# Optimization experiments

Hardware: AMD Instinct MI355X
Metric: run time of the kernel (lower is better)

Reference implementation:

```python
import jax, jax.numpy as jnp
import numpy as np

B, M, K = 32768, 8192, 16
EPS = 1e-5  # torch BatchNorm1d default


def _bn_relu(x, g, b):
    # training-mode batch norm (biased variance), matching torch BatchNorm1d forward
    m = x.mean(0)
    v = x.var(0)
    return jax.nn.relu(g * (x - m) * jax.lax.rsqrt(v + EPS) + b)


def _forward(pos, mc, mv, w1, b1, w2, b2, w3, b3, w4, b4, w5, b5, w6, b6,
             g1, be1, g2, be2, g3, be3, g4, be4, g5, be5, k):
    # squared pairwise distances [B, M]; same ordering as L2 norm used by torch.sort
    d2 = (pos * pos).sum(1, keepdims=True) + (mc * mc).sum(1)[None, :] - 2.0 * (pos @ mc.T)
    _, idx = jax.lax.top_k(-d2, k)                     # k nearest indices [B, k]
    nb = jnp.concatenate([mc[idx], mv[idx]], axis=-1)  # [B, k, 4] = (coord, value) per neighbor
    knn_feat = jnp.concatenate([pos, nb.reshape(pos.shape[0], k * 4)], axis=1)  # [B, 2+4k]
    x = _bn_relu(knn_feat @ w1 + b1, g1, be1)
    x = _bn_relu(x @ w2 + b2, g2, be2)
    x = _bn_relu(x @ w3 + b3, g3, be3)
    x = _bn_relu(x @ w4 + b4, g4, be4)
    x = _bn_relu(x @ w5 + b5, g5, be5)  # dropout = identity (eval mode)
    x = x @ w6 + b6
    return x, knn_feat


def setup_inputs() -> dict:
    key = jax.random.key(0)
    ks = jax.random.split(key, 32)
    d_in = 2 + K * 4
    dims = [(d_in, 128), (128, 256), (256, 512), (512, 128), (128, 64), (64, 2)]
    inp = {
        "pos": jax.random.normal(ks[0], (B, 2), jnp.float32),
        "measure_coords": jax.random.normal(ks[1], (M, 2), jnp.float32),
        "measure_vals": jax.random.normal(ks[2], (M, 2), jnp.float32),
    }
    for i, (fi, fo) in enumerate(dims, 1):
        inp[f"w{i}"] = jax.random.normal(ks[2 + 2 * i], (fi, fo), jnp.float32) / np.float32(np.sqrt(fi))
        inp[f"b{i}"] = jnp.zeros((fo,), jnp.float32)
    for i, n in enumerate([128, 256, 512, 128, 64], 1):
        inp[f"g{i}"] = jnp.ones((n,), jnp.float32)
        inp[f"be{i}"] = jnp.zeros((n,), jnp.float32)
    inp["k"] = K
    return inp


def reference(pos, measure_coords, measure_vals, w1, b1, w2, b2, w3, b3, w4, b4,
              w5, b5, w6, b6, g1, be1, g2, be2, g3, be3, g4, be4, g5, be5, k):
    return _forward(pos, measure_coords, measure_vals, w1, b1, w2, b2, w3, b3, w4,
                    b4, w5, b5, w6, b6, g1, be1, g2, be2, g3, be3, g4, be4, g5, be5, k)
```

## Files before the change

kernel.cpp:

```cpp
#include <hip/hip_runtime.h>

typedef unsigned short u16;
typedef unsigned int   u32;
typedef __attribute__((ext_vector_type(8))) short bf16x8;
typedef __attribute__((ext_vector_type(4))) float f32x4;

#define B_ROWS 32768
#define EPS_BN 1e-5f

__device__ __forceinline__ u16 f2bf(float f) {
  u32 u = __float_as_uint(f);
  u32 r = (u + 0x7FFFu + ((u >> 16) & 1u)) >> 16;
  return (u16)r;
}
__device__ __forceinline__ float bf2f(u16 h) {
  return __uint_as_float(((u32)h) << 16);
}

__device__ __forceinline__ float dcalc(float px, float py, float sp, float mx, float my) {
#pragma clang fp contract(off)
  float sm   = mx * mx + my * my;
  float pm   = px * mx;
  float dot  = __builtin_fmaf(py, my, pm);
  float spsm = sp + sm;
  return __builtin_fmaf(dot, -2.0f, spsm);
}
__device__ __forceinline__ float dcalc2(float px, float py, float sp, float mx, float my,
                                        float sm) {
#pragma clang fp contract(off)
  float pm   = px * mx;
  float dot  = __builtin_fmaf(py, my, pm);
  float spsm = sp + sm;
  return __builtin_fmaf(dot, -2.0f, spsm);
}
__device__ __forceinline__ float smcalc(float mx, float my) {
#pragma clang fp contract(off)
  return mx * mx + my * my;
}
__device__ __forceinline__ float spcalc(float px, float py) {
#pragma clang fp contract(off)
  return px * px + py * py;
}
#define MED3 __builtin_amdgcn_fmed3f

__device__ __forceinline__ int nth_set_bit(unsigned long long m, int n) {
  u32 w = (u32)m;
  int base = 0;
  int c = __popc(w);
  if (n >= c) { n -= c; w = (u32)(m >> 32); base = 32; }
  int p = __popc(w & 0xFFFFu); if (n >= p) { n -= p; w >>= 16; base += 16; }
  p = __popc(w & 0xFFu);       if (n >= p) { n -= p; w >>= 8;  base += 8; }
  p = __popc(w & 0xFu);        if (n >= p) { n -= p; w >>= 4;  base += 4; }
  p = __popc(w & 0x3u);        if (n >= p) { n -= p; w >>= 2;  base += 2; }
  p = (int)(w & 1u);           if (n >= p) { base += 1; }
  return base;
}

__device__ __forceinline__ float sel8(const float a[8], int j) {
  float x01 = (j & 1) ? a[1] : a[0];
  float x23 = (j & 1) ? a[3] : a[2];
  float x45 = (j & 1) ? a[5] : a[4];
  float x67 = (j & 1) ? a[7] : a[6];
  float xl  = (j & 2) ? x23 : x01;
  float xh  = (j & 2) ? x67 : x45;
  return (j & 4) ? xh : xl;
}

__global__ __launch_bounds__(256, 4)
void knn_kernel(const float2* __restrict__ pos, const float2* __restrict__ mc,
                const float2* __restrict__ mv, float* __restrict__ knn_out,
                u16* __restrict__ X0)
{
  __shared__ float tv[32 * 130];
  __shared__ float tstS[32];
  __shared__ int   qcnt[32];

  const int t = threadIdx.x;
  const int g = t >> 6;
  const int s = t & 63;
  const int q0 = blockIdx.x * 32;

  float px[8], py[8], sp[8];
#pragma unroll
  for (int j = 0; j < 8; ++j) {
    float2 p = pos[q0 + g * 8 + j];
    px[j] = p.x; py[j] = p.y; sp[j] = spcalc(p.x, p.y);
  }

  const float4* mc4 = (const float4*)mc;
  const int b4 = s * 64;

  float z0[8], z1[8];
#pragma unroll
  for (int j = 0; j < 8; ++j) { z0[j] = __builtin_inff(); z1[j] = __builtin_inff(); }

  float4 cur = mc4[b4];
  for (int i = 0; i < 64; ++i) {
    float4 nxt = mc4[b4 + ((i + 1) & 63)];
    float smA = smcalc(cur.x, cur.y);
    float smB = smcalc(cur.z, cur.w);
#pragma unroll
    for (int j = 0; j < 8; ++j) {
      float dA = dcalc2(px[j], py[j], sp[j], cur.x, cur.y, smA);
      z1[j] = MED3(z0[j], dA, z1[j]); z0[j] = fminf(z0[j], dA);
      float dB = dcalc2(px[j], py[j], sp[j], cur.z, cur.w, smB);
      z1[j] = MED3(z0[j], dB, z1[j]); z0[j] = fminf(z0[j], dB);
    }
    cur = nxt;
  }
#pragma unroll
  for (int j = 0; j < 8; ++j) {
    float2 zz; zz.x = z0[j]; zz.y = z1[j];
    *(float2*)(&tv[(g * 8 + j) * 130 + s * 2]) = zz;
  }
  __syncthreads();

  if (t < 32) {
    float ch[16];
#pragma unroll
    for (int j = 0; j < 16; ++j) ch[j] = __builtin_inff();
    for (int k = 0; k < 128; ++k) {
      float v = tv[t * 130 + k];
#pragma unroll
      for (int j = 15; j >= 1; --j) ch[j] = MED3(ch[j-1], v, ch[j]);
      ch[0] = fminf(ch[0], v);
    }
    tstS[t] = ch[15];
    qcnt[t] = 0;
  }
  __syncthreads();
  float Tq[8];
#pragma unroll
  for (int j = 0; j < 8; ++j) Tq[j] = tstS[g * 8 + j];
  __syncthreads();

  unsigned long long am[8];
#pragma unroll
  for (int j = 0; j < 8; ++j) am[j] = __ballot(z0[j] <= Tq[j]);
  int total = 0;
#pragma unroll
  for (int j = 0; j < 8; ++j) total += __popcll(am[j]);

  u16* qcand = (u16*)tv;
  for (int t0 = s; t0 < total; t0 += 64) {
    int rem = t0, jq = 0, sl = -1;
#pragma unroll
    for (int jj = 0; jj < 8; ++jj) {
      if (sl < 0) {
        int c = __popcll(am[jj]);
        if (rem < c) { sl = nth_set_bit(am[jj], rem); jq = jj; }
        else rem -= c;
      }
    }
    float qx = sel8(px, jq), qy = sel8(py, jq);
    float qs = sel8(sp, jq), qT = sel8(Tq, jq);
    const int qrow = g * 8 + jq;
    const int bpt = sl * 128;
    const float4* mbase = mc4 + sl * 64;
#pragma unroll 4
    for (int i = 0; i < 64; ++i) {
      float4 c2 = mbase[i];
      float smA = smcalc(c2.x, c2.y);
      float smB = smcalc(c2.z, c2.w);
      float dA = dcalc2(qx, qy, qs, c2.x, c2.y, smA);
      float dB = dcalc2(qx, qy, qs, c2.z, c2.w, smB);
      if (dA <= qT) {
        int o = atomicAdd(&qcnt[qrow], 1);
        if (o < 64) qcand[qrow * 64 + o] = (u16)(bpt + 2 * i);
      }
      if (dB <= qT) {
        int o = atomicAdd(&qcnt[qrow], 1);
        if (o < 64) qcand[qrow * 64 + o] = (u16)(bpt + 2 * i + 1);
      }
    }
  }
  __syncthreads();

  if (t < 32) {
    const int q = q0 + t;
    float2 p = pos[q];
    const float sq = spcalc(p.x, p.y);
    int cnt = qcnt[t]; if (cnt > 64) cnt = 64;
    float fd[16]; int fi[16];
#pragma unroll
    for (int j = 0; j < 16; ++j) { fd[j] = __builtin_inff(); fi[j] = 0x7fffffff; }
    for (int j = 0; j < cnt; ++j) {
      int ci = qcand[t * 64 + j];
      float2 m = mc[ci];
      float d = dcalc(p.x, p.y, sq, m.x, m.y);
      bool cc = (d < fd[15]) || (d == fd[15] && ci < fi[15]);
      if (cc) {
#pragma unroll
        for (int k = 15; k >= 1; --k) {
          bool cm = (d < fd[k-1]) || (d == fd[k-1] && ci < fi[k-1]);
          if (cc) {
            if (cm) { fd[k] = fd[k-1]; fi[k] = fi[k-1]; }
            else    { fd[k] = d;       fi[k] = ci;      }
          }
          cc = cm;
        }
        if (cc) { fd[0] = d; fi[0] = ci; }
      }
    }
    float* orow = knn_out + (size_t)q * 66;
    u16*   xrow = X0 + (size_t)q * 96;
    orow[0] = p.x; orow[1] = p.y;
    xrow[0] = f2bf(p.x); xrow[1] = f2bf(p.y);
#pragma unroll
    for (int j = 0; j < 16; ++j) {
      int ci = fi[j];
      float2 m = mc[ci], v = mv[ci];
      orow[2 + 4*j + 0] = m.x; orow[2 + 4*j + 1] = m.y;
      orow[2 + 4*j + 2] = v.x; orow[2 + 4*j + 3] = v.y;
      xrow[2 + 4*j + 0] = f2bf(m.x); xrow[2 + 4*j + 1] = f2bf(m.y);
      xrow[2 + 4*j + 2] = f2bf(v.x); xrow[2 + 4*j + 3] = f2bf(v.y);
    }
#pragma unroll
    for (int c = 66; c < 96; ++c) xrow[c] = 0;
  }
}

__global__ __launch_bounds__(256)
void prep_wt_all(const float* __restrict__ w1, const float* __restrict__ w2,
                 const float* __restrict__ w3, const float* __restrict__ w4,
                 const float* __restrict__ w5,
                 u16* __restrict__ wt1, u16* __restrict__ wt2, u16* __restrict__ wt3,
                 u16* __restrict__ wt4, u16* __restrict__ wt5)
{
  const int l = blockIdx.y;
  const float* w; u16* wt; int K, N, Kp;
  if (l == 0)      { w = w1; wt = wt1; K = 66;  N = 128; Kp = 96;  }
  else if (l == 1) { w = w2; wt = wt2; K = 128; N = 256; Kp = 128; }
  else if (l == 2) { w = w3; wt = wt3; K = 256; N = 512; Kp = 256; }
  else if (l == 3) { w = w4; wt = wt4; K = 512; N = 128; Kp = 512; }
  else             { w = w5; wt = wt5; K = 128; N = 64;  Kp = 128; }
  int i = blockIdx.x * 256 + threadIdx.x;
  if (i >= N * Kp) return;
  int n = i / Kp, kp = i - n * Kp;
  float v = (kp < K) ? w[(size_t)kp * N + n] : 0.0f;
  wt[i] = f2bf(v);
}

template<int BN, bool FUSE>
__global__ __launch_bounds__(256)
void gemm_bn_kernel(const u16* __restrict__ X, int Kw,
                    const u16* __restrict__ WT,
                    const float* __restrict__ bias,
                    const float* __restrict__ psum, const float* __restrict__ psq,
                    const float* __restrict__ gw,   const float* __restrict__ bw,
                    u16* __restrict__ Z, int N,
                    float* __restrict__ csum, float* __restrict__ csq)
{
  constexpr int BM = 128;
  constexpr int AST = 40;
  __shared__ u16 Ash[BM * AST];
  __shared__ u16 Bsh[BN * AST];
  __shared__ float redS[4][BN];
  __shared__ float redQ[4][BN];
  __shared__ float scA[512];
  __shared__ float ttA[512];

  const int t = threadIdx.x;
  const int wave = t >> 6;
  const int lane = t & 63;
  const int lr = lane & 15;
  const int qd = lane >> 4;
  const int m0 = blockIdx.x * BM;
  const int n0 = blockIdx.y * BN;

  if (FUSE) {
    const float invB = 1.0f / 32768.0f;
    for (int c = t; c < Kw; c += 256) {
      float mean = psum[c] * invB;
      float var  = __fmaf_rn(-mean, mean, psq[c] * invB);
      float sc   = gw[c] * rsqrtf(var + EPS_BN);
      scA[c] = sc;
      ttA[c] = __fmaf_rn(-mean, sc, bw[c]);
    }
    __syncthreads();
  }

  f32x4 acc[2][BN / 16];
#pragma unroll
  for (int a = 0; a < 2; ++a)
#pragma unroll
    for (int b = 0; b < BN / 16; ++b) {
      acc[a][b][0] = 0.f; acc[a][b][1] = 0.f; acc[a][b][2] = 0.f; acc[a][b][3] = 0.f;
    }

  const int sr = t >> 2;
  const int sk = (t & 3) * 8;

  for (int k0 = 0; k0 < Kw; k0 += 32) {
#pragma unroll
    for (int rr = 0; rr < 2; ++rr) {
      int r = sr + rr * 64;
      uint4 g = *(const uint4*)(&X[(size_t)(m0 + r) * Kw + k0 + sk]);
      if (FUSE) {
        u32 w[4] = {g.x, g.y, g.z, g.w};
        u32 o[4];
#pragma unroll
        for (int e = 0; e < 4; ++e) {
          int kk = k0 + sk + 2 * e;
          float lo = bf2f((u16)(w[e] & 0xffffu));
          float hi = bf2f((u16)(w[e] >> 16));
          float yl = fmaxf(__fmaf_rn(lo, scA[kk],     ttA[kk]),     0.0f);
          float yh = fmaxf(__fmaf_rn(hi, scA[kk + 1], ttA[kk + 1]), 0.0f);
          o[e] = (u32)f2bf(yl) | ((u32)f2bf(yh) << 16);
        }
        g.x = o[0]; g.y = o[1]; g.z = o[2]; g.w = o[3];
      }
      *(uint4*)(&Ash[r * AST + sk]) = g;
    }
    if (BN == 128) {
#pragma unroll
      for (int rr = 0; rr < 2; ++rr) {
        int n = sr + rr * 64;
        *(uint4*)(&Bsh[n * AST + sk]) =
            *(const uint4*)(&WT[(size_t)(n0 + n) * Kw + k0 + sk]);
      }
    } else {
      int n = sr;
      *(uint4*)(&Bsh[n * AST + sk]) =
          *(const uint4*)(&WT[(size_t)(n0 + n) * Kw + k0 + sk]);
    }
    __syncthreads();
    bf16x8 af0 = *(const bf16x8*)(&Ash[(wave * 32 + lr) * AST + qd * 8]);
    bf16x8 af1 = *(const bf16x8*)(&Ash[(wave * 32 + 16 + lr) * AST + qd * 8]);
#pragma unroll
    for (int ct = 0; ct < BN / 16; ++ct) {
      bf16x8 bfr = *(const bf16x8*)(&Bsh[(ct * 16 + lr) * AST + qd * 8]);
      acc[0][ct] = __builtin_amdgcn_mfma_f32_16x16x32_bf16(af0, bfr, acc[0][ct], 0, 0, 0);
      acc[1][ct] = __builtin_amdgcn_mfma_f32_16x16x32_bf16(af1, bfr, acc[1][ct], 0, 0, 0);
    }
    __syncthreads();
  }

#pragma unroll
  for (int ct = 0; ct < BN / 16; ++ct) {
    int cg = n0 + ct * 16 + lr;
    float bv = bias[cg];
    float s = 0.f, sqv = 0.f;
#pragma unroll
    for (int rt = 0; rt < 2; ++rt) {
#pragma unroll
      for (int r = 0; r < 4; ++r) {
        float z = acc[rt][ct][r] + bv;
        int row = m0 + wave * 32 + rt * 16 + qd * 4 + r;
        Z[(size_t)row * N + cg] = f2bf(z);
        s += z;
        sqv = __fmaf_rn(z, z, sqv);
      }
    }
    s   += __shfl_xor(s, 16);   s   += __shfl_xor(s, 32);
    sqv += __shfl_xor(sqv, 16); sqv += __shfl_xor(sqv, 32);
    if (qd == 0) { redS[wave][ct * 16 + lr] = s; redQ[wave][ct * 16 + lr] = sqv; }
  }
  __syncthreads();
  if (t < BN) {
    float s  = redS[0][t] + redS[1][t] + redS[2][t] + redS[3][t];
    float sv = redQ[0][t] + redQ[1][t] + redQ[2][t] + redQ[3][t];
    atomicAdd(&csum[n0 + t], s);
    atomicAdd(&csq[n0 + t], sv);
  }
}

__global__ __launch_bounds__(256)
void gemv6_kernel(const u16* __restrict__ Z5, const float* __restrict__ w6,
                  const float* __restrict__ b6,
                  const float* __restrict__ psum, const float* __restrict__ psq,
                  const float* __restrict__ gw,   const float* __restrict__ bw,
                  float* __restrict__ out)
{
  __shared__ float wsh[128];
  __shared__ float scs[64];
  __shared__ float tts[64];
  const int t = threadIdx.x;
  if (t < 128) wsh[t] = w6[t];
  if (t < 64) {
    const float invB = 1.0f / 32768.0f;
    float mean = psum[t] * invB;
    float var  = __fmaf_rn(-mean, mean, psq[t] * invB);
    float sc   = gw[t] * rsqrtf(var + EPS_BN);
    scs[t] = sc;
    tts[t] = __fmaf_rn(-mean, sc, bw[t]);
  }
  __syncthreads();
  const int q = blockIdx.x * 256 + t;
  const uint4* xv = (const uint4*)(Z5 + (size_t)q * 64);
  float a0 = 0.f, a1 = 0.f;
#pragma unroll
  for (int cc = 0; cc < 8; ++cc) {
    uint4 pk = xv[cc];
    u32 u[4] = {pk.x, pk.y, pk.z, pk.w};
#pragma unroll
    for (int uu = 0; uu < 4; ++uu) {
      int k = cc * 8 + uu * 2;
      float z0 = bf2f((u16)(u[uu] & 0xffffu));
      float z1 = bf2f((u16)(u[uu] >> 16));
      float x0 = fmaxf(__fmaf_rn(z0, scs[k],     tts[k]),     0.0f);
      float x1 = fmaxf(__fmaf_rn(z1, scs[k + 1], tts[k + 1]), 0.0f);
      x0 = bf2f(f2bf(x0));
      x1 = bf2f(f2bf(x1));
      a0 = __fmaf_rn(x0, wsh[2 * k + 0], a0);
      a1 = __fmaf_rn(x0, wsh[2 * k + 1], a1);
      a0 = __fmaf_rn(x1, wsh[2 * k + 2], a0);
      a1 = __fmaf_rn(x1, wsh[2 * k + 3], a1);
    }
  }
  float2 o; o.x = a0 + b6[0]; o.y = a1 + b6[1];
  ((float2*)out)[q] = o;
}

extern "C" void kernel_launch(void* const* d_in, const int* in_sizes, int n_in,
                              void* d_out, int out_size, void* d_ws, size_t ws_size,
                              hipStream_t stream)
{
  const float2* pos = (const float2*)d_in[0];
  const float2* mc  = (const float2*)d_in[1];
  const float2* mv  = (const float2*)d_in[2];
  const float* w1 = (const float*)d_in[3];  const float* b1 = (const float*)d_in[4];
  const float* w2 = (const float*)d_in[5];  const float* b2 = (const float*)d_in[6];
  const float* w3 = (const float*)d_in[7];  const float* b3 = (const float*)d_in[8];
  const float* w4 = (const float*)d_in[9];  const float* b4 = (const float*)d_in[10];
  const float* w5 = (const float*)d_in[11]; const float* b5 = (const float*)d_in[12];
  const float* w6 = (const float*)d_in[13]; const float* b6 = (const float*)d_in[14];
  const float* g1 = (const float*)d_in[15]; const float* be1 = (const float*)d_in[16];
  const float* g2 = (const float*)d_in[17]; const float* be2 = (const float*)d_in[18];
  const float* g3 = (const float*)d_in[19]; const float* be3 = (const float*)d_in[20];
  const float* g4 = (const float*)d_in[21]; const float* be4 = (const float*)d_in[22];
  const float* g5 = (const float*)d_in[23]; const float* be5 = (const float*)d_in[24];

  char* ws = (char*)d_ws;
  u16* X0   = (u16*)(ws + 0);
  u16* ZA   = (u16*)(ws + 6291456);
  u16* ZB   = (u16*)(ws + 39845888);
  u16* WT1  = (u16*)(ws + 73400320);
  u16* WT2  = (u16*)(ws + 73424896);
  u16* WT3  = (u16*)(ws + 73490432);
  u16* WT4  = (u16*)(ws + 73752576);
  u16* WT5  = (u16*)(ws + 73883648);
  float* stats = (float*)(ws + 73900032);
  float* s1 = stats;        float* s2 = stats + 128;  float* s3 = stats + 384;
  float* s4 = stats + 896;  float* s5 = stats + 1024;
  float* sqb = stats + 1088;
  float* q1 = sqb;          float* q2 = sqb + 128;    float* q3 = sqb + 384;
  float* q4 = sqb + 896;    float* q5 = sqb + 1024;

  float* outX = (float*)d_out;
  float* outK = outX + 2 * B_ROWS;

  hipMemsetAsync(stats, 0, 2176 * sizeof(float), stream);
  prep_wt_all<<<dim3(512, 5), 256, 0, stream>>>(w1, w2, w3, w4, w5, WT1, WT2, WT3, WT4, WT5);
  knn_kernel<<<dim3(1024), 256, 0, stream>>>(pos, mc, mv, outK, X0);

  gemm_bn_kernel<64, false><<<dim3(256, 2), 256, 0, stream>>>(
      X0, 96, WT1, b1, nullptr, nullptr, nullptr, nullptr, ZA, 128, s1, q1);
  gemm_bn_kernel<64, true><<<dim3(256, 4), 256, 0, stream>>>(
      ZA, 128, WT2, b2, s1, q1, g1, be1, ZB, 256, s2, q2);
  gemm_bn_kernel<64, true><<<dim3(256, 8), 256, 0, stream>>>(
      ZB, 256, WT3, b3, s2, q2, g2, be2, ZA, 512, s3, q3);
  gemm_bn_kernel<64, true><<<dim3(256, 2), 256, 0, stream>>>(
      ZA, 512, WT4, b4, s3, q3, g3, be3, ZB, 128, s4, q4);
  gemm_bn_kernel<64, true><<<dim3(256, 1), 256, 0, stream>>>(
      ZB, 128, WT5, b5, s4, q4, g4, be4, ZA, 64, s5, q5);
  gemv6_kernel<<<dim3(128), 256, 0, stream>>>(ZA, w6, b6, s5, q5, g5, be5, outX);

  (void)in_sizes; (void)n_in; (void)out_size; (void)ws_size;
}
```

Baseline: 354.3 us.

## Flatten candidate-slice rescan tasks into a block-wide shared-memory task list

Replaces the per-wavefront enumeration of candidate (query, slice) pairs, which decoded each task with popcount and nth-set-bit searches, with a shared task list. Each query writes its ballot mask to shared memory, 32 threads expand the masks into packed u16 tasks, and all 256 threads then pull tasks from that list. The aim is to balance the rescan work across the four wavefronts and drop the per-task bit-decoding overhead. In exchange it adds extra shared-memory traffic, an atomic, and a serial expansion loop run by 32 threads.

```diff
diff --git a/kernel.cpp b/kernel.cpp
--- a/kernel.cpp
+++ b/kernel.cpp
@@ -43,29 +43,6 @@
 }
 #define MED3 __builtin_amdgcn_fmed3f
 
-__device__ __forceinline__ int nth_set_bit(unsigned long long m, int n) {
-  u32 w = (u32)m;
-  int base = 0;
-  int c = __popc(w);
-  if (n >= c) { n -= c; w = (u32)(m >> 32); base = 32; }
-  int p = __popc(w & 0xFFFFu); if (n >= p) { n -= p; w >>= 16; base += 16; }
-  p = __popc(w & 0xFFu);       if (n >= p) { n -= p; w >>= 8;  base += 8; }
-  p = __popc(w & 0xFu);        if (n >= p) { n -= p; w >>= 4;  base += 4; }
-  p = __popc(w & 0x3u);        if (n >= p) { n -= p; w >>= 2;  base += 2; }
-  p = (int)(w & 1u);           if (n >= p) { base += 1; }
-  return base;
-}
-
-__device__ __forceinline__ float sel8(const float a[8], int j) {
-  float x01 = (j & 1) ? a[1] : a[0];
-  float x23 = (j & 1) ? a[3] : a[2];
-  float x45 = (j & 1) ? a[5] : a[4];
-  float x67 = (j & 1) ? a[7] : a[6];
-  float xl  = (j & 2) ? x23 : x01;
-  float xh  = (j & 2) ? x67 : x45;
-  return (j & 4) ? xh : xl;
-}
-
 __global__ __launch_bounds__(256, 4)
 void knn_kernel(const float2* __restrict__ pos, const float2* __restrict__ mc,
                 const float2* __restrict__ mv, float* __restrict__ knn_out,
@@ -73,7 +50,10 @@
 {
   __shared__ float tv[32 * 130];
   __shared__ float tstS[32];
+  __shared__ float qxS[32], qyS[32], qsS[32];
+  __shared__ unsigned long long qmaskS[32];
   __shared__ int   qcnt[32];
+  __shared__ int   ntaskS;
 
   const int t = threadIdx.x;
   const int g = t >> 6;
@@ -85,6 +65,10 @@
   for (int j = 0; j < 8; ++j) {
     float2 p = pos[q0 + g * 8 + j];
     px[j] = p.x; py[j] = p.y; sp[j] = spcalc(p.x, p.y);
+  }
+#pragma unroll
+  for (int j = 0; j < 8; ++j) {
+    if (s == j) { qxS[g * 8 + j] = px[j]; qyS[g * 8 + j] = py[j]; qsS[g * 8 + j] = sp[j]; }
   }
 
   const float4* mc4 = (const float4*)mc;
@@ -127,36 +111,47 @@
     }
     tstS[t] = ch[15];
     qcnt[t] = 0;
-  }
-  __syncthreads();
-  float Tq[8];
-#pragma unroll
-  for (int j = 0; j < 8; ++j) Tq[j] = tstS[g * 8 + j];
-  __syncthreads();
-
-  unsigned long long am[8];
-#pragma unroll
-  for (int j = 0; j < 8; ++j) am[j] = __ballot(z0[j] <= Tq[j]);
-  int total = 0;
-#pragma unroll
-  for (int j = 0; j < 8; ++j) total += __popcll(am[j]);
+    if (t == 0) ntaskS = 0;
+  }
+  __syncthreads();
+
+  {
+    float Tq[8];
+#pragma unroll
+    for (int j = 0; j < 8; ++j) Tq[j] = tstS[g * 8 + j];
+    unsigned long long m;
+#pragma unroll
+    for (int j = 0; j < 8; ++j) {
+      m = __ballot(z0[j] <= Tq[j]);
+      if (s == j) qmaskS[g * 8 + j] = m;
+    }
+  }
+  __syncthreads();
 
   u16* qcand = (u16*)tv;
-  for (int t0 = s; t0 < total; t0 += 64) {
-    int rem = t0, jq = 0, sl = -1;
-#pragma unroll
-    for (int jj = 0; jj < 8; ++jj) {
-      if (sl < 0) {
-        int c = __popcll(am[jj]);
-        if (rem < c) { sl = nth_set_bit(am[jj], rem); jq = jj; }
-        else rem -= c;
-      }
-    }
-    float qx = sel8(px, jq), qy = sel8(py, jq);
-    float qs = sel8(sp, jq), qT = sel8(Tq, jq);
-    const int qrow = g * 8 + jq;
+  u16* taskS = ((u16*)tv) + 2048;
+  if (t < 32) {
+    unsigned long long m = qmaskS[t];
+    int c = __popcll(m);
+    int off = atomicAdd(&ntaskS, c);
+    u16 qb = (u16)(t << 6);
+    while (m) {
+      int b = (int)__builtin_ctzll(m);
+      m &= m - 1;
+      taskS[off++] = qb | (u16)b;
+    }
+  }
+  __syncthreads();
+
+  const int ntask = ntaskS;
+  for (int i0 = t; i0 < ntask; i0 += 256) {
+    const int task = taskS[i0];
+    const int qrow = task >> 6;
+    const int sl   = task & 63;
+    const float qx = qxS[qrow], qy = qyS[qrow];
+    const float qs = qsS[qrow], qT = tstS[qrow];
+    const float4* mbase = mc4 + sl * 64;
     const int bpt = sl * 128;
-    const float4* mbase = mc4 + sl * 64;
 #pragma unroll 4
     for (int i = 0; i < 64; ++i) {
       float4 c2 = mbase[i];
```

After: 342.2 us. -3.4%, faster.
